# Performance work log

Measured on AMD Instinct MI355X. Metric: run time of the kernel, lower is better.

## Reference

```python
import jax, jax.numpy as jnp
import numpy as np

ROPE_BASE = 10000.0

def _rope(x):
    # x: (B, S, D); canonical interleaved RoPE over sequence positions
    B, S, D = x.shape
    half = D // 2
    inv_freq = 1.0 / (ROPE_BASE ** (jnp.arange(half, dtype=x.dtype) * 2.0 / D))  # (half,)
    ang = jnp.arange(S, dtype=x.dtype)[:, None] * inv_freq[None, :]              # (S, half)
    cos, sin = jnp.cos(ang), jnp.sin(ang)
    x1 = x[..., 0::2]   # (B, S, half)
    x2 = x[..., 1::2]
    rot = jnp.stack([x1 * cos - x2 * sin, x1 * sin + x2 * cos], axis=-1)         # (B,S,half,2)
    return rot.reshape(B, S, D)

def setup_inputs() -> dict:
    key = jax.random.key(0)
    ks = jax.random.split(key, 7)
    B, S, D = 32, 1024, 768
    sc = 1.0 / np.sqrt(D)
    return {
        "x":  jax.random.normal(ks[0], (B, S, D), dtype=jnp.float32),
        "Wq": jax.random.normal(ks[1], (D, D), dtype=jnp.float32) * sc,
        "bq": jax.random.normal(ks[2], (D,), dtype=jnp.float32) * 0.01,
        "Wk": jax.random.normal(ks[3], (D, D), dtype=jnp.float32) * sc,
        "bk": jax.random.normal(ks[4], (D,), dtype=jnp.float32) * 0.01,
        "Wv": jax.random.normal(ks[5], (D, D), dtype=jnp.float32) * sc,
        "bv": jax.random.normal(ks[6], (D,), dtype=jnp.float32) * 0.01,
    }

def reference(x, Wq, bq, Wk, bk, Wv, bv):
    D = x.shape[-1]
    # torch nn.Linear: y = x @ W.T + b
    Q = jnp.einsum('bsd,ed->bse', x, Wq) + bq
    K = jnp.einsum('bsd,ed->bse', x, Wk) + bk
    V = jnp.einsum('bsd,ed->bse', x, Wv) + bv
    Q = _rope(Q)
    K = _rope(K)
    scores = jnp.einsum('bqd,bkd->bqk', Q, K) / jnp.sqrt(jnp.asarray(D, x.dtype))
    weights = jax.nn.softmax(scores, axis=-1)
    return jnp.einsum('bqk,bkd->bqd', weights, V)
```

## Files before the change

### kernel.cpp

```cpp
#include <hip/hip_runtime.h>


typedef __attribute__((ext_vector_type(8))) _Float16 f16x8;
typedef __attribute__((ext_vector_type(4))) float    f32x4;

__device__ __forceinline__ unsigned short f2h(float f) {
    _Float16 h = (_Float16)f;
    return __builtin_bit_cast(unsigned short, h);
}
__device__ __forceinline__ float h2f(unsigned short u) {
    return (float)__builtin_bit_cast(_Float16, u);
}

__device__ __forceinline__ void async_ld16(const void* g, void* l) {
    __builtin_amdgcn_global_load_lds(
        (const __attribute__((address_space(1))) void*)g,
        (__attribute__((address_space(3))) void*)l, 16, 0, 0);
}

template<int MODE, int KDIM, int LDA, int LDB>
__global__ __launch_bounds__(256)
void gemm_bt(const unsigned short* __restrict__ A,
             const unsigned short* __restrict__ B,
             void* __restrict__ C0, void* __restrict__ C1,
             const float* __restrict__ bias0,
             const float* __restrict__ bias1,
             float scale)
{
    __shared__ __align__(16) unsigned short sA[128 * 64];
    __shared__ __align__(16) unsigned short sB[128 * 64];

    const int tid  = threadIdx.x;
    const int lane = tid & 63;
    const int wave = tid >> 6;
    const int wrow = (wave >> 1) * 64;
    const int wcol = (wave & 1) * 64;
    const int quad = lane >> 4;
    const int l15  = lane & 15;

    int m0, n0, z = 0;
    if constexpr (MODE == 0) {
        m0 = (blockIdx.x & 255) * 128;  n0 = (blockIdx.x >> 8) * 128;
    } else if constexpr (MODE == 1) {
        n0 = (blockIdx.x & 255) * 128;  m0 = (blockIdx.x >> 8) * 128;
    } else if constexpr (MODE == 2) {
        z = blockIdx.x & 31; const int q = blockIdx.x >> 5;
        m0 = (q >> 3) * 128; n0 = (q & 7) * 128;
    } else {
        z = blockIdx.x & 31; const int q = blockIdx.x >> 5;
        m0 = (q / 6) * 128;  n0 = (q % 6) * 128;
    }

    const unsigned short* Ab = A;
    const unsigned short* Bb = B;
    if constexpr (MODE == 2) { Ab += (size_t)z * 786432;  Bb += (size_t)z * 786432; }
    if constexpr (MODE == 3) { Ab += (size_t)z * 1048576; Bb += (size_t)z * 786432; }

    const int srow = tid >> 3;
    const int sk   = ((tid & 7) ^ (srow & 7)) * 8;

    f32x4 acc[4][4] = {};

    for (int kt = 0; kt < KDIM; kt += 64) {
        __syncthreads();
        #pragma unroll
        for (int g = 0; g < 4; ++g) {
            async_ld16(Ab + (size_t)(m0 + g * 32 + srow) * LDA + kt + sk,
                       &sA[g * 2048 + tid * 8]);
            async_ld16(Bb + (size_t)(n0 + g * 32 + srow) * LDB + kt + sk,
                       &sB[g * 2048 + tid * 8]);
        }
        __syncthreads();

        #pragma unroll
        for (int kk = 0; kk < 2; ++kk) {
            f16x8 af[4], bfr[4];
            #pragma unroll
            for (int mi = 0; mi < 4; ++mi) {
                const int r = wrow + mi * 16 + l15;
                af[mi] = *(const f16x8*)&sA[r * 64 + (((kk * 4 + quad) ^ (r & 7)) << 3)];
            }
            #pragma unroll
            for (int ni = 0; ni < 4; ++ni) {
                const int r = wcol + ni * 16 + l15;
                bfr[ni] = *(const f16x8*)&sB[r * 64 + (((kk * 4 + quad) ^ (r & 7)) << 3)];
            }
            #pragma unroll
            for (int mi = 0; mi < 4; ++mi)
                #pragma unroll
                for (int ni = 0; ni < 4; ++ni)
                    acc[mi][ni] = __builtin_amdgcn_mfma_f32_16x16x32_f16(
                        af[mi], bfr[ni], acc[mi][ni], 0, 0, 0);
        }
    }

    const bool evenlane = (l15 & 1) == 0;

    float invf[4];
    if constexpr (MODE == 0) {
        #pragma unroll
        for (int ni = 0; ni < 4; ++ni) {
            int col = n0 + wcol + ni * 16 + l15;
            if (col >= 768) col -= 768;
            invf[ni] = exp2f((float)(col >> 1) * -0.03460341765507773f);
        }
    }

    #pragma unroll
    for (int mi = 0; mi < 4; ++mi) {
        #pragma unroll
        for (int ni = 0; ni < 4; ++ni) {
            #pragma unroll
            for (int reg = 0; reg < 4; ++reg) {
                const int grow = m0 + wrow + mi * 16 + quad * 4 + reg;
                const int gcol = n0 + wcol + ni * 16 + l15;
                float v = acc[mi][ni][reg];
                if constexpr (MODE == 0) {
                    const bool isQ = gcol < 768;
                    const int  col = isQ ? gcol : gcol - 768;
                    v += isQ ? bias0[col] : bias1[col];
                    const float other = __shfl_xor(v, 1);
                    const int   s     = grow & 1023;
                    const float ang   = (float)s * invf[ni];
                    float sn, cs;
                    __sincosf(ang, &sn, &cs);
                    float r = (col & 1) ? fmaf(other, sn, v * cs)
                                        : fmaf(v, cs, -(other * sn));
                    if (isQ) r *= scale;
                    const unsigned short h = f2h(r);
                    const unsigned int packed =
                        (unsigned int)h | (__shfl_xor((unsigned int)h, 1) << 16);
                    if (evenlane) {
                        unsigned short* dst = (unsigned short*)(isQ ? C0 : C1);
                        *(unsigned int*)(dst + (size_t)grow * 768 + col) = packed;
                    }
                } else if constexpr (MODE == 1) {
                    v += bias0[grow];
                    const unsigned short h = f2h(v);
                    const unsigned int packed =
                        (unsigned int)h | (__shfl_xor((unsigned int)h, 1) << 16);
                    if (evenlane) {
                        const int b = gcol >> 10, s = gcol & 1023;
                        *(unsigned int*)((unsigned short*)C0 + (size_t)b * (768 * 1024)
                                         + (size_t)grow * 1024 + s) = packed;
                    }
                } else if constexpr (MODE == 2) {
                    const unsigned short h = f2h(v);
                    const unsigned int packed =
                        (unsigned int)h | (__shfl_xor((unsigned int)h, 1) << 16);
                    if (evenlane) {
                        *(unsigned int*)((unsigned short*)C0 + (size_t)z * 1048576
                                         + (size_t)grow * 1024 + gcol) = packed;
                    }
                } else {
                    const float vo = __shfl_xor(v, 1);
                    if (evenlane) {
                        float2 p; p.x = v; p.y = vo;
                        *(float2*)(((float*)C0) + (size_t)z * 786432
                                   + (size_t)grow * 768 + gcol) = p;
                    }
                }
            }
        }
    }
}

__global__ __launch_bounds__(256)
void softmax_rows(const unsigned short* __restrict__ S, unsigned short* __restrict__ P)
{
    const int row = blockIdx.x;
    const int tid = threadIdx.x;
    const ushort4 u = ((const ushort4*)(S + (size_t)row * 1024))[tid];
    const float v0 = h2f(u.x), v1 = h2f(u.y), v2 = h2f(u.z), v3 = h2f(u.w);

    float m = fmaxf(fmaxf(v0, v1), fmaxf(v2, v3));
    #pragma unroll
    for (int o = 1; o < 64; o <<= 1) m = fmaxf(m, __shfl_xor(m, o));
    __shared__ float redm[4];
    __shared__ float reds[4];
    const int wave = tid >> 6, lane = tid & 63;
    if (lane == 0) redm[wave] = m;
    __syncthreads();
    m = fmaxf(fmaxf(redm[0], redm[1]), fmaxf(redm[2], redm[3]));

    const float e0 = __expf(v0 - m), e1 = __expf(v1 - m);
    const float e2 = __expf(v2 - m), e3 = __expf(v3 - m);
    float sum = e0 + e1 + e2 + e3;
    #pragma unroll
    for (int o = 1; o < 64; o <<= 1) sum += __shfl_xor(sum, o);
    if (lane == 0) reds[wave] = sum;
    __syncthreads();
    sum = reds[0] + reds[1] + reds[2] + reds[3];
    const float inv = 1.0f / sum;

    ushort4 o4;
    o4.x = f2h(e0 * inv); o4.y = f2h(e1 * inv);
    o4.z = f2h(e2 * inv); o4.w = f2h(e3 * inv);
    ((ushort4*)(P + (size_t)row * 1024))[tid] = o4;
}

__global__ void cvt_f32_f16(const float4* __restrict__ in,
                            ushort4* __restrict__ out, int n4)
{
    int i = blockIdx.x * 256 + threadIdx.x;
    const int stride = gridDim.x * 256;
    for (; i < n4; i += stride) {
        const float4 v = in[i];
        ushort4 o;
        o.x = f2h(v.x); o.y = f2h(v.y); o.z = f2h(v.z); o.w = f2h(v.w);
        out[i] = o;
    }
}

extern "C" void kernel_launch(void* const* d_in, const int* in_sizes, int n_in,
                              void* d_out, int out_size, void* d_ws, size_t ws_size,
                              hipStream_t stream)
{
    const float* x  = (const float*)d_in[0];
    const float* Wq = (const float*)d_in[1];
    const float* bq = (const float*)d_in[2];
    const float* Wk = (const float*)d_in[3];
    const float* bk = (const float*)d_in[4];
    const float* Wv = (const float*)d_in[5];
    const float* bv = (const float*)d_in[6];
    float* out = (float*)d_out;

    char* ws = (char*)d_ws;
    unsigned short* xh  = (unsigned short*)(ws + 0);
    unsigned short* wqk = (unsigned short*)(ws + 50331648);
    unsigned short* wvh = (unsigned short*)(ws + 52690944);
    unsigned short* Qh  = (unsigned short*)(ws + 53870592);
    unsigned short* Kh  = (unsigned short*)(ws + 104202240);
    unsigned short* Vt  = (unsigned short*)(ws + 154533888);
    unsigned short* Sc  = (unsigned short*)(ws + 204865536);
    unsigned short* Ph  = (unsigned short*)(ws + 0);

    cvt_f32_f16<<<4096, 256, 0, stream>>>((const float4*)x,  (ushort4*)xh, 25165824 / 4);
    cvt_f32_f16<<<576,  256, 0, stream>>>((const float4*)Wq, (ushort4*)wqk, 589824 / 4);
    cvt_f32_f16<<<576,  256, 0, stream>>>((const float4*)Wk, (ushort4*)(wqk + 589824), 589824 / 4);
    cvt_f32_f16<<<576,  256, 0, stream>>>((const float4*)Wv, (ushort4*)wvh, 589824 / 4);

    const float qscale = 0.03608439182435161f;

    gemm_bt<0, 768, 768, 768><<<3072, 256, 0, stream>>>(
        xh, wqk, Qh, Kh, bq, bk, qscale);
    gemm_bt<1, 768, 768, 768><<<1536, 256, 0, stream>>>(
        wvh, xh, Vt, nullptr, bv, nullptr, 1.0f);
    gemm_bt<2, 768, 768, 768><<<2048, 256, 0, stream>>>(
        Qh, Kh, Sc, nullptr, nullptr, nullptr, 1.0f);
    softmax_rows<<<32768, 256, 0, stream>>>(Sc, Ph);
    gemm_bt<3, 1024, 1024, 1024><<<1536, 256, 0, stream>>>(
        Ph, Vt, out, nullptr, nullptr, nullptr, 1.0f);
}
```

Before: 571.1 us.

## Use 256x256 GEMM tiles with double-buffered LDS pipeline and XCD-aware block mapping

```diff
diff --git a/kernel.cpp b/kernel.cpp
--- a/kernel.cpp
+++ b/kernel.cpp
@@ -19,7 +19,7 @@
 }
 
 template<int MODE, int KDIM, int LDA, int LDB>
-__global__ __launch_bounds__(256)
+__global__ __launch_bounds__(512, 2)
 void gemm_bt(const unsigned short* __restrict__ A,
              const unsigned short* __restrict__ B,
              void* __restrict__ C0, void* __restrict__ C1,
@@ -27,28 +27,32 @@
              const float* __restrict__ bias1,
              float scale)
 {
-    __shared__ __align__(16) unsigned short sA[128 * 64];
-    __shared__ __align__(16) unsigned short sB[128 * 64];
+    __shared__ __align__(16) unsigned short sA[2][256 * 64];
+    __shared__ __align__(16) unsigned short sB[2][256 * 64];
 
     const int tid  = threadIdx.x;
     const int lane = tid & 63;
     const int wave = tid >> 6;
-    const int wrow = (wave >> 1) * 64;
-    const int wcol = (wave & 1) * 64;
+    const int wm   = wave >> 2;
+    const int wn   = wave & 3;
+    const int wrow = wm * 128;
+    const int wcol = wn * 64;
     const int quad = lane >> 4;
     const int l15  = lane & 15;
 
+    const int xcd = blockIdx.x & 7;
+    const int bi  = blockIdx.x >> 3;
     int m0, n0, z = 0;
     if constexpr (MODE == 0) {
-        m0 = (blockIdx.x & 255) * 128;  n0 = (blockIdx.x >> 8) * 128;
+        m0 = (xcd * 16 + bi / 6) * 256;  n0 = (bi % 6) * 256;
     } else if constexpr (MODE == 1) {
-        n0 = (blockIdx.x & 255) * 128;  m0 = (blockIdx.x >> 8) * 128;
+        n0 = (xcd * 16 + bi / 3) * 256;  m0 = (bi % 3) * 256;
     } else if constexpr (MODE == 2) {
-        z = blockIdx.x & 31; const int q = blockIdx.x >> 5;
-        m0 = (q >> 3) * 128; n0 = (q & 7) * 128;
+        z = xcd * 4 + bi / 16; const int t = bi % 16;
+        m0 = (t >> 2) * 256; n0 = (t & 3) * 256;
     } else {
-        z = blockIdx.x & 31; const int q = blockIdx.x >> 5;
-        m0 = (q / 6) * 128;  n0 = (q % 6) * 128;
+        z = xcd * 4 + bi / 12; const int t = bi % 12;
+        m0 = (t / 3) * 256;  n0 = (t % 3) * 256;
     }
 
     const unsigned short* Ab = A;
@@ -58,40 +62,93 @@
 
     const int srow = tid >> 3;
     const int sk   = ((tid & 7) ^ (srow & 7)) * 8;
-
-    f32x4 acc[4][4] = {};
-
-    for (int kt = 0; kt < KDIM; kt += 64) {
-        __syncthreads();
-        #pragma unroll
-        for (int g = 0; g < 4; ++g) {
-            async_ld16(Ab + (size_t)(m0 + g * 32 + srow) * LDA + kt + sk,
-                       &sA[g * 2048 + tid * 8]);
-            async_ld16(Bb + (size_t)(n0 + g * 32 + srow) * LDB + kt + sk,
-                       &sB[g * 2048 + tid * 8]);
-        }
-        __syncthreads();
-
-        #pragma unroll
-        for (int kk = 0; kk < 2; ++kk) {
-            f16x8 af[4], bfr[4];
-            #pragma unroll
-            for (int mi = 0; mi < 4; ++mi) {
-                const int r = wrow + mi * 16 + l15;
-                af[mi] = *(const f16x8*)&sA[r * 64 + (((kk * 4 + quad) ^ (r & 7)) << 3)];
-            }
+    const int sdst = (tid & 7) * 8;
+
+    auto stgA = [&](int buf, int r0, int kt) {
+        async_ld16(Ab + (size_t)(m0 + r0 + srow) * LDA + kt + sk,
+                   &sA[buf][(r0 + srow) * 64 + sdst]);
+    };
+    auto stgB = [&](int buf, int r0, int kt) {
+        async_ld16(Bb + (size_t)(n0 + r0 + srow) * LDB + kt + sk,
+                   &sB[buf][(r0 + srow) * 64 + sdst]);
+    };
+
+    f32x4 acc[8][4] = {};
+
+    constexpr int NT = KDIM / 64;
+
+    stgA(0, 0, 0); stgA(0, 128, 0); stgB(0, 0, 0); stgB(0, 64, 0);
+    stgA(0, 64, 0); stgA(0, 192, 0); stgB(0, 128, 0); stgB(0, 192, 0);
+    stgA(1, 0, 64); stgA(1, 128, 64); stgB(1, 0, 64); stgB(1, 64, 64);
+    stgA(1, 64, 64); stgA(1, 192, 64); stgB(1, 128, 64); stgB(1, 192, 64);
+    asm volatile("s_waitcnt vmcnt(8)" ::: "memory");
+    __builtin_amdgcn_s_barrier();
+
+    int p = 0;
+    #pragma unroll 2
+    for (int t = 0; t < NT; ++t, p ^= 1) {
+        const int  kt2  = (t + 2) * 64;
+        const bool pref = (t + 2) < NT;
+        const unsigned short* sAp = sA[p];
+        const unsigned short* sBp = sB[p];
+
+        f16x8 bfr[4][2], af[4][2];
+        #pragma unroll
+        for (int ni = 0; ni < 4; ++ni) {
+            const int r = wcol + ni * 16 + l15;
+            const int x = r & 7;
+            bfr[ni][0] = *(const f16x8*)&sBp[r * 64 + ((quad       ^ x) << 3)];
+            bfr[ni][1] = *(const f16x8*)&sBp[r * 64 + (((4 + quad) ^ x) << 3)];
+        }
+        #pragma unroll
+        for (int mi = 0; mi < 4; ++mi) {
+            const int r = wrow + mi * 16 + l15;
+            const int x = r & 7;
+            af[mi][0] = *(const f16x8*)&sAp[r * 64 + ((quad       ^ x) << 3)];
+            af[mi][1] = *(const f16x8*)&sAp[r * 64 + (((4 + quad) ^ x) << 3)];
+        }
+        asm volatile("s_waitcnt lgkmcnt(0)" ::: "memory");
+        __builtin_amdgcn_s_barrier();
+        if (pref) { stgA(p, 0, kt2); stgA(p, 128, kt2);
+                    stgB(p, 0, kt2); stgB(p, 64, kt2); }
+        __builtin_amdgcn_s_setprio(1);
+        #pragma unroll
+        for (int mi = 0; mi < 4; ++mi)
             #pragma unroll
             for (int ni = 0; ni < 4; ++ni) {
-                const int r = wcol + ni * 16 + l15;
-                bfr[ni] = *(const f16x8*)&sB[r * 64 + (((kk * 4 + quad) ^ (r & 7)) << 3)];
+                acc[mi][ni] = __builtin_amdgcn_mfma_f32_16x16x32_f16(
+                    af[mi][0], bfr[ni][0], acc[mi][ni], 0, 0, 0);
+                acc[mi][ni] = __builtin_amdgcn_mfma_f32_16x16x32_f16(
+                    af[mi][1], bfr[ni][1], acc[mi][ni], 0, 0, 0);
             }
+        __builtin_amdgcn_s_setprio(0);
+
+        #pragma unroll
+        for (int mi = 0; mi < 4; ++mi) {
+            const int r = wrow + 64 + mi * 16 + l15;
+            const int x = r & 7;
+            af[mi][0] = *(const f16x8*)&sAp[r * 64 + ((quad       ^ x) << 3)];
+            af[mi][1] = *(const f16x8*)&sAp[r * 64 + (((4 + quad) ^ x) << 3)];
+        }
+        asm volatile("s_waitcnt lgkmcnt(0)" ::: "memory");
+        __builtin_amdgcn_s_barrier();
+        if (pref) { stgA(p, 64, kt2); stgA(p, 192, kt2);
+                    stgB(p, 128, kt2); stgB(p, 192, kt2); }
+        __builtin_amdgcn_s_setprio(1);
+        #pragma unroll
+        for (int mi = 0; mi < 4; ++mi)
             #pragma unroll
-            for (int mi = 0; mi < 4; ++mi)
-                #pragma unroll
-                for (int ni = 0; ni < 4; ++ni)
-                    acc[mi][ni] = __builtin_amdgcn_mfma_f32_16x16x32_f16(
-                        af[mi], bfr[ni], acc[mi][ni], 0, 0, 0);
-        }
+            for (int ni = 0; ni < 4; ++ni) {
+                acc[4 + mi][ni] = __builtin_amdgcn_mfma_f32_16x16x32_f16(
+                    af[mi][0], bfr[ni][0], acc[4 + mi][ni], 0, 0, 0);
+                acc[4 + mi][ni] = __builtin_amdgcn_mfma_f32_16x16x32_f16(
+                    af[mi][1], bfr[ni][1], acc[4 + mi][ni], 0, 0, 0);
+            }
+        __builtin_amdgcn_s_setprio(0);
+
+        if (pref) asm volatile("s_waitcnt vmcnt(8)" ::: "memory");
+        else      asm volatile("s_waitcnt vmcnt(0)" ::: "memory");
+        __builtin_amdgcn_s_barrier();
     }
 
     const bool evenlane = (l15 & 1) == 0;
@@ -107,12 +164,13 @@
     }
 
     #pragma unroll
-    for (int mi = 0; mi < 4; ++mi) {
+    for (int mi = 0; mi < 8; ++mi) {
+        const int rowoff = (mi & 3) * 16 + (mi >> 2) * 64;
         #pragma unroll
         for (int ni = 0; ni < 4; ++ni) {
             #pragma unroll
             for (int reg = 0; reg < 4; ++reg) {
-                const int grow = m0 + wrow + mi * 16 + quad * 4 + reg;
+                const int grow = m0 + wrow + rowoff + quad * 4 + reg;
                 const int gcol = n0 + wcol + ni * 16 + l15;
                 float v = acc[mi][ni][reg];
                 if constexpr (MODE == 0) {
@@ -155,9 +213,9 @@
                 } else {
                     const float vo = __shfl_xor(v, 1);
                     if (evenlane) {
-                        float2 p; p.x = v; p.y = vo;
+                        float2 pk; pk.x = v; pk.y = vo;
                         *(float2*)(((float*)C0) + (size_t)z * 786432
-                                   + (size_t)grow * 768 + gcol) = p;
+                                   + (size_t)grow * 768 + gcol) = pk;
                     }
                 }
             }
@@ -242,13 +300,13 @@
 
     const float qscale = 0.03608439182435161f;
 
-    gemm_bt<0, 768, 768, 768><<<3072, 256, 0, stream>>>(
+    gemm_bt<0, 768, 768, 768><<<768, 512, 0, stream>>>(
         xh, wqk, Qh, Kh, bq, bk, qscale);
-    gemm_bt<1, 768, 768, 768><<<1536, 256, 0, stream>>>(
+    gemm_bt<1, 768, 768, 768><<<384, 512, 0, stream>>>(
         wvh, xh, Vt, nullptr, bv, nullptr, 1.0f);
-    gemm_bt<2, 768, 768, 768><<<2048, 256, 0, stream>>>(
+    gemm_bt<2, 768, 768, 768><<<512, 512, 0, stream>>>(
         Qh, Kh, Sc, nullptr, nullptr, nullptr, 1.0f);
     softmax_rows<<<32768, 256, 0, stream>>>(Sc, Ph);
-    gemm_bt<3, 1024, 1024, 1024><<<1536, 256, 0, stream>>>(
+    gemm_bt<3, 1024, 1024, 1024><<<384, 512, 0, stream>>>(
         Ph, Vt, out, nullptr, nullptr, nullptr, 1.0f);
 }
```

Result: faster. 521.6 us (-8.7%).
